# Kernel optimization log

Hardware: AMD Instinct MI355X
Metric: run time of the kernel (lower is better)

Reference implementation:

```python
import jax, jax.numpy as jnp
import numpy as np

UNITS = 512
D_Q = 1024
D_V = 1024


def setup_inputs() -> dict:
    key = jax.random.key(0)
    ks = jax.random.split(key, 12)
    B, L = 32, 2048
    inp = {
        "query": jax.random.normal(ks[0], (B, D_Q), jnp.float32),
        "values": jax.random.normal(ks[1], (B, L, D_V), jnp.float32),
        "mask": jnp.zeros((B, L, 1), jnp.float32),
        "previous_scores": jax.random.uniform(ks[2], (B, L, 1), jnp.float32),
        "timestep": 3,
        # Dense params (glorot-ish scale)
        "Wh": jax.random.normal(ks[3], (D_Q, UNITS), jnp.float32) / np.sqrt(D_Q),
        "bh": jnp.zeros((UNITS,), jnp.float32),
        "Wv": jax.random.normal(ks[4], (D_V, UNITS), jnp.float32) / np.sqrt(D_V),
        "bv": jnp.zeros((UNITS,), jnp.float32),
        "Wp": jax.random.normal(ks[5], (3, UNITS), jnp.float32) / np.sqrt(3.0),
        "bp": jnp.zeros((UNITS,), jnp.float32),
        "Wm": jax.random.normal(ks[6], (5, UNITS), jnp.float32) / np.sqrt(5.0),
        "bm": jnp.zeros((UNITS,), jnp.float32),
        "vw": jax.random.normal(ks[7], (UNITS, 1), jnp.float32) / np.sqrt(UNITS),
        "vb": jnp.zeros((1,), jnp.float32),
    }
    return inp


def reference(query, values, mask, previous_scores, timestep,
              Wh, bh, Wv, bv, Wp, bp, Wm, bm, vw, vb):
    B, L, _ = mask.shape
    # input_lengths: 1 + count of mask==0 along seq, tiled across L  -> [B, L, 1]
    input_len = 1.0 + jnp.sum((mask == 0).astype(jnp.float32), axis=1)  # [B, 1]
    input_len = jnp.broadcast_to(input_len, (B, L))[..., None]          # [B, L, 1]
    # positional features: [1+timestep, 2+pos, input_len], logged -> [B, L, 3]
    pos2 = jnp.stack([jnp.full((L,), 1.0 + timestep, jnp.float32),
                      2.0 + jnp.arange(L, dtype=jnp.float32)], axis=-1)  # [L, 2]
    pos2 = jnp.broadcast_to(pos2[None], (B, L, 2))
    positional = jnp.log(jnp.concatenate([pos2, input_len], axis=-1))    # [B, L, 3]
    # markov: sliding window of width 5 over zero-padded previous scores -> [B, L, 5]
    padded = jnp.pad(previous_scores[:, :, 0], ((0, 0), (2, 2)))         # [B, L+4]
    widx = jnp.arange(L)[:, None] + jnp.arange(5)[None, :]               # [L, 5]
    markov = padded[:, widx]                                             # [B, L, 5]
    # additive attention score
    summand = (jnp.einsum('bq,qu->bu', query, Wh) + bh)[:, None, :]      # [B, 1, U]
    summand = summand + (jnp.einsum('blv,vu->blu', values, Wv) + bv)
    summand = summand + (jnp.einsum('blp,pu->blu', positional, Wp) + bp)
    summand = summand + (jnp.einsum('blm,mu->blu', markov, Wm) + bm)
    score = jnp.einsum('blu,uo->blo', jnp.tanh(summand), vw) + vb        # [B, L, 1]
    score = score + mask * (-1e9)
    attention_weights = jax.nn.softmax(score, axis=1)                    # [B, L, 1]
    context_vector = jnp.sum(attention_weights * values, axis=1)         # [B, D_V]
    return (context_vector, attention_weights)
```

## Files before the change

kernel.cpp:

```cpp
#include <hip/hip_runtime.h>
#include <hip/hip_bf16.h>
#include <math.h>

#define NB 32
#define LL 2048
#define DV 1024
#define NU 512
#define NM (NB * LL)

typedef __attribute__((ext_vector_type(8))) short short8;
typedef __attribute__((ext_vector_type(4))) float f32x4;

#define GLL16(g, l)                                                            \
  __builtin_amdgcn_global_load_lds(                                            \
      (const __attribute__((address_space(1))) void*)(g),                      \
      (__attribute__((address_space(3))) void*)(l), 16, 0, 0)

__device__ __forceinline__ float fast_tanh(float x) {
  x = fminf(fmaxf(x, -15.f), 15.f);
  float e = __expf(2.f * x);
  return (e - 1.f) / (e + 1.f);
}

__global__ __launch_bounds__(256) void prep_kernel(
    const float* __restrict__ Wv, __hip_bfloat16* __restrict__ wvpk,
    const float* __restrict__ q, const float* __restrict__ Wh,
    const float* __restrict__ bh, const float* __restrict__ bv,
    const float* __restrict__ bp, const float* __restrict__ bm,
    const float* __restrict__ Wp, const int* __restrict__ ts,
    const float* __restrict__ mask, float* __restrict__ h) {
  if (blockIdx.x < 64) {
    int t = blockIdx.x * 256 + threadIdx.x;
    int u4 = t & 127;
    int kg = t >> 7;
    int k0 = kg * 8;
    int kt = kg >> 2;
    int qd = kg & 3;
    float4 f[8];
#pragma unroll
    for (int j = 0; j < 8; j++)
      f[j] = *(const float4*)(Wv + (size_t)(k0 + j) * NU + u4 * 4);
#pragma unroll
    for (int e = 0; e < 4; e++) {
      int u = u4 * 4 + e;
      int nt = u >> 8, n = u & 255;
      int c = qd ^ ((n >> 1) & 3);
      int idx = nt * 32768 + kt * 1024 + n * 4 + c;
      const float* fe = (const float*)&f[0] + e;
      union {
        __hip_bfloat162 h2[4];
        int4 v;
      } pk;
#pragma unroll
      for (int m = 0; m < 4; m++)
        pk.h2[m] =
            __float22bfloat162_rn(make_float2(fe[(2 * m) * 4], fe[(2 * m + 1) * 4]));
      ((int4*)wvpk)[idx] = pk.v;
    }
    return;
  }
  int idx2 = blockIdx.x - 64;
  int u0 = (idx2 & 7) * 64;
  int bq = idx2 >> 3;
  int tid = threadIdx.x;

  __shared__ float qsL[8][1024];
  __shared__ float cnt[8], lgl[8];

  {
    int g = tid & 31, bl = tid >> 5;
    const float4* mrow =
        (const float4*)(mask + (size_t)(bq * 8 + bl) * LL) + g * 16;
    float c = 0.f;
#pragma unroll
    for (int j = 0; j < 16; j++) {
      float4 m = mrow[j];
      c += (m.x == 0.f ? 1.f : 0.f) + (m.y == 0.f ? 1.f : 0.f) +
           (m.z == 0.f ? 1.f : 0.f) + (m.w == 0.f ? 1.f : 0.f);
    }
#pragma unroll
    for (int o = 16; o >= 1; o >>= 1) c += __shfl_xor(c, o, 64);
    if (g == 0) cnt[bl] = c;
  }
  __syncthreads();
  if (tid < 8) lgl[tid] = logf(1.f + cnt[tid]);

#pragma unroll
  for (int j = 0; j < 8; j++) {
    int f = j * 256 + tid;
    int bl = f >> 8, k4 = f & 255;
    *(float4*)&qsL[bl][k4 * 4] =
        *(const float4*)(q + (size_t)(bq * 8 + bl) * 1024 + k4 * 4);
  }
  __syncthreads();

  int u = tid & 63, bsub = tid >> 6;
  int b0 = bq * 8 + bsub * 2, b1 = b0 + 1;
  float a0e = 0.f, a0o = 0.f, a1e = 0.f, a1o = 0.f;
#pragma unroll 16
  for (int k = 0; k < 1024; k += 2) {
    float w0 = Wh[(size_t)k * NU + u0 + u];
    float w1 = Wh[(size_t)(k + 1) * NU + u0 + u];
    a0e += w0 * qsL[bsub * 2][k];
    a1e += w0 * qsL[bsub * 2 + 1][k];
    a0o += w1 * qsL[bsub * 2][k + 1];
    a1o += w1 * qsL[bsub * 2 + 1][k + 1];
  }
  float acc0 = a0e + a0o, acc1 = a1e + a1o;

  int uu = u0 + u;
  float lt = logf(1.0f + (float)ts[0]);
  float bias = bh[uu] + bv[uu] + bp[uu] + bm[uu] + lt * Wp[uu];
  float wp2 = Wp[2 * NU + uu];
  h[b0 * NU + uu] = acc0 + bias + lgl[bsub * 2] * wp2;
  h[b1 * NU + uu] = acc1 + bias + lgl[bsub * 2 + 1] * wp2;
}

__global__ __launch_bounds__(512, 4) void score_kernel(
    const float* __restrict__ values, const __hip_bfloat16* __restrict__ wvpk,
    const float* __restrict__ h, const float* __restrict__ Wp,
    const float* __restrict__ Wm, const float* __restrict__ vw,
    const float* __restrict__ prev, float* __restrict__ partial) {
  int lin = blockIdx.x;
  int group = lin >> 4, sub = lin & 15;
  int ntile = sub >> 3;
  int mtile = group * 8 + (sub & 7);
  int tid = threadIdx.x;
  int lane = tid & 63, wid = tid >> 6;
  int wr = wid >> 2, wc = wid & 3;
  int col = lane & 15, quad = lane >> 4;
  int b = mtile >> 4;
  int l0 = (mtile & 15) << 7;
  int rowbase = mtile << 7;

  __shared__ __align__(16) char AsB[2][8192];
  __shared__ __align__(16) char BsB[2][16384];
  __shared__ float hL[256], wp1L[256], vwL[256], wmL[5][256];
  __shared__ float loglS[128], prevs[132], scoreAcc[128];

  if (tid < 256) {
    int u = ntile * 256 + tid;
    hL[tid] = h[b * NU + u];
    wp1L[tid] = Wp[NU + u];
    vwL[tid] = vw[u];
#pragma unroll
    for (int j = 0; j < 5; j++) wmL[j][tid] = Wm[j * NU + u];
  }
  if (tid < 128) {
    loglS[tid] = __logf(2.0f + (float)(l0 + tid));
    scoreAcc[tid] = 0.f;
  }
  if (tid < 132) {
    int li = l0 - 2 + tid;
    prevs[tid] = (li >= 0 && li < LL) ? prev[(size_t)b * LL + li] : 0.f;
  }

  f32x4 acc[4][4];
  f32x4 zero4 = {0.f, 0.f, 0.f, 0.f};
#pragma unroll
  for (int i = 0; i < 4; i++)
#pragma unroll
    for (int j = 0; j < 4; j++) acc[i][j] = zero4;

  int row = tid >> 2, h0 = tid & 3;
  const float* abase = values + (size_t)(rowbase + row) * DV + h0 * 8;
  int s_sw = (row >> 1) & 3;
  int aoff = row * 64 + ((h0 ^ s_sw) * 16);
  const char* bbase = (const char*)wvpk + (size_t)ntile * 32 * 16384;
  int boff = tid * 16;

  float4 preA[2][2];

#define CVT_STORE(SLOT, DSTBUF)                                                \
  {                                                                            \
    float4 f0 = preA[SLOT][0], f1 = preA[SLOT][1];                             \
    union {                                                                    \
      __hip_bfloat162 h2[4];                                                   \
      int4 v;                                                                  \
    } pk;                                                                      \
    pk.h2[0] = __float22bfloat162_rn(make_float2(f0.x, f0.y));                 \
    pk.h2[1] = __float22bfloat162_rn(make_float2(f0.z, f0.w));                 \
    pk.h2[2] = __float22bfloat162_rn(make_float2(f1.x, f1.y));                 \
    pk.h2[3] = __float22bfloat162_rn(make_float2(f1.z, f1.w));                 \
    *(int4*)(AsB[DSTBUF] + aoff) = pk.v;                                       \
  }

  {
#pragma unroll
    for (int d = 0; d < 2; d++) {
      preA[d][0] = *(const float4*)(abase + d * 32);
      preA[d][1] = *(const float4*)(abase + d * 32 + 4);
    }
    GLL16(bbase + boff, BsB[0] + boff);
    GLL16(bbase + boff + 8192, BsB[0] + boff + 8192);
    CVT_STORE(0, 0);
    preA[0][0] = *(const float4*)(abase + 2 * 32);
    preA[0][1] = *(const float4*)(abase + 2 * 32 + 4);
    __syncthreads();
  }

#define KSTEP(KT, CBUF, OSLOT, DO_STAGE, DO_RELOAD)                            \
  {                                                                            \
    if (DO_STAGE) {                                                            \
      const char* bsrc = bbase + (size_t)((KT) + 1) * 16384;                   \
      GLL16(bsrc + boff, BsB[(CBUF) ^ 1] + boff);                              \
      GLL16(bsrc + boff + 8192, BsB[(CBUF) ^ 1] + boff + 8192);                \
      CVT_STORE(OSLOT, (CBUF) ^ 1);                                            \
      if (DO_RELOAD) {                                                         \
        preA[OSLOT][0] = *(const float4*)(abase + ((KT) + 3) * 32);            \
        preA[OSLOT][1] = *(const float4*)(abase + ((KT) + 3) * 32 + 4);        \
      }                                                                        \
    }                                                                          \
    short8 aF[4];                                                              \
    _Pragma("unroll") for (int t = 0; t < 4; t++) {                            \
      int m = wr * 64 + t * 16 + col;                                          \
      aF[t] = *(const short8*)(AsB[CBUF] + m * 64 +                            \
                               ((quad ^ ((m >> 1) & 3)) * 16));                \
    }                                                                          \
    _Pragma("unroll") for (int tc = 0; tc < 4; tc++) {                         \
      int n = wc * 64 + tc * 16 + col;                                         \
      short8 bF =                                                              \
          *(const short8*)(BsB[CBUF] + n * 64 + ((quad ^ ((n >> 1) & 3)) * 16)); \
      _Pragma("unroll") for (int tr = 0; tr < 4; tr++) acc[tr][tc] =           \
          __builtin_amdgcn_mfma_f32_16x16x32_bf16(aF[tr], bF, acc[tr][tc], 0,  \
                                                  0, 0);                       \
    }                                                                          \
    __syncthreads();                                                           \
  }

  for (int kto = 0; kto < 14; kto++) {
    KSTEP(2 * kto, 0, 1, 1, 1);
    KSTEP(2 * kto + 1, 1, 0, 1, 1);
  }
  KSTEP(28, 0, 1, 1, 1);
  KSTEP(29, 1, 0, 1, 0);
  KSTEP(30, 0, 1, 1, 0);
  KSTEP(31, 1, 0, 0, 0);
#undef KSTEP
#undef CVT_STORE

  int rb = wr * 64;
#pragma unroll
  for (int tr = 0; tr < 4; tr++) {
    float ps[4] = {0.f, 0.f, 0.f, 0.f};
#pragma unroll
    for (int tc = 0; tc < 4; tc++) {
      int uc = wc * 64 + tc * 16 + col;
      float hh = hL[uc], wp1 = wp1L[uc], vv = vwL[uc];
      float m0 = wmL[0][uc], m1 = wmL[1][uc], m2 = wmL[2][uc],
            m3 = wmL[3][uc], m4 = wmL[4][uc];
      int r0 = rb + tr * 16 + quad * 4;
#pragma unroll
      for (int i = 0; i < 4; i++) {
        int r = r0 + i;
        float e = hh + loglS[r] * wp1 + prevs[r] * m0 + prevs[r + 1] * m1 +
                  prevs[r + 2] * m2 + prevs[r + 3] * m3 + prevs[r + 4] * m4;
        float sv = acc[tr][tc][i] + e;
        ps[i] += fast_tanh(sv) * vv;
      }
    }
#pragma unroll
    for (int i = 0; i < 4; i++) {
      float v = ps[i];
      v += __shfl_xor(v, 1, 64);
      v += __shfl_xor(v, 2, 64);
      v += __shfl_xor(v, 4, 64);
      v += __shfl_xor(v, 8, 64);
      if (col == 0) atomicAdd(&scoreAcc[rb + tr * 16 + quad * 4 + i], v);
    }
  }
  __syncthreads();
  if (tid < 128)
    partial[(size_t)ntile * NM + rowbase + tid] = scoreAcc[tid];
}

__global__ __launch_bounds__(1024) void post_kernel(
    const float* __restrict__ partial, const float* __restrict__ mask,
    const float* __restrict__ values, float* __restrict__ aw,
    float* __restrict__ out) {
  int b = blockIdx.x >> 3, chunk = blockIdx.x & 7;
  int tid = threadIdx.x;
  int lane = tid & 63, wid = tid >> 6;
  __shared__ float wmx[16], wsm[16];
  __shared__ float awL[256];
  __shared__ f32x4 red[4][256];

  size_t base = (size_t)b * LL;
  float s1, s2;
  {
    size_t l1 = base + tid, l2 = base + tid + 1024;
    s1 = partial[l1] + partial[(size_t)NM + l1] + mask[l1] * -1.0e9f;
    s2 = partial[l2] + partial[(size_t)NM + l2] + mask[l2] * -1.0e9f;
  }
  float mx = fmaxf(s1, s2);
#pragma unroll
  for (int o = 32; o >= 1; o >>= 1) mx = fmaxf(mx, __shfl_xor(mx, o, 64));
  if (lane == 0) wmx[wid] = mx;
  __syncthreads();
  mx = wmx[0];
#pragma unroll
  for (int j = 1; j < 16; j++) mx = fmaxf(mx, wmx[j]);
  float e = __expf(s1 - mx) + __expf(s2 - mx);
#pragma unroll
  for (int o = 32; o >= 1; o >>= 1) e += __shfl_xor(e, o, 64);
  if (lane == 0) wsm[wid] = e;
  __syncthreads();
  float sum = 0.f;
#pragma unroll
  for (int j = 0; j < 16; j++) sum += wsm[j];
  float inv = 1.0f / sum;

  int l0 = chunk * 256;
  if (tid < 256) {
    size_t l = base + l0 + tid;
    float s = partial[l] + partial[(size_t)NM + l] + mask[l] * -1.0e9f;
    float a = __expf(s - mx) * inv;
    aw[l] = a;
    awL[tid] = a;
  }
  __syncthreads();

  int s = tid & 255, rg = tid >> 8;
  const float4* vbase =
      (const float4*)(values + ((size_t)b * LL + l0 + rg * 64) * DV) + s;
  const float* awr = awL + rg * 64;
  float4 acc = make_float4(0.f, 0.f, 0.f, 0.f);
  for (int i0 = 0; i0 < 64; i0 += 8) {
    float4 v[8];
#pragma unroll
    for (int j = 0; j < 8; j++) v[j] = vbase[(size_t)(i0 + j) * 256];
#pragma unroll
    for (int j = 0; j < 8; j++) {
      float w = awr[i0 + j];
      acc.x += w * v[j].x;
      acc.y += w * v[j].y;
      acc.z += w * v[j].z;
      acc.w += w * v[j].w;
    }
  }
  f32x4 a4 = {acc.x, acc.y, acc.z, acc.w};
  red[rg][s] = a4;
  __syncthreads();
  if (tid < 256) {
    f32x4 r = red[0][s];
    f32x4 r1 = red[1][s], r2 = red[2][s], r3 = red[3][s];
    r += r1;
    r += r2;
    r += r3;
    float* o = out + (size_t)b * DV + s * 4;
    atomicAdd(o + 0, r[0]);
    atomicAdd(o + 1, r[1]);
    atomicAdd(o + 2, r[2]);
    atomicAdd(o + 3, r[3]);
  }
}

extern "C" void kernel_launch(void* const* d_in, const int* in_sizes, int n_in,
                              void* d_out, int out_size, void* d_ws,
                              size_t ws_size, hipStream_t stream) {
  const float* query = (const float*)d_in[0];
  const float* values = (const float*)d_in[1];
  const float* mask = (const float*)d_in[2];
  const float* prev = (const float*)d_in[3];
  const int* ts = (const int*)d_in[4];
  const float* Wh = (const float*)d_in[5];
  const float* bh = (const float*)d_in[6];
  const float* Wv = (const float*)d_in[7];
  const float* bv = (const float*)d_in[8];
  const float* Wp = (const float*)d_in[9];
  const float* bp = (const float*)d_in[10];
  const float* Wm = (const float*)d_in[11];
  const float* bm = (const float*)d_in[12];
  const float* vw = (const float*)d_in[13];

  float* out = (float*)d_out;
  float* ws = (float*)d_ws;
  float* h = ws + 1024;
  float* partial = ws + 32768;
  __hip_bfloat16* wvpk =
      (__hip_bfloat16*)((char*)d_ws + (size_t)163840 * 4);
  float* aw = out + 32768;

  hipMemsetAsync(d_out, 0, 32768 * sizeof(float), stream);
  prep_kernel<<<96, 256, 0, stream>>>(Wv, wvpk, query, Wh, bh, bv, bp, bm, Wp,
                                      ts, mask, h);
  score_kernel<<<1024, 512, 0, stream>>>(values, wvpk, h, Wp, Wm, vw, prev,
                                         partial);
  post_kernel<<<256, 1024, 0, stream>>>(partial, mask, values, aw, out);
}
```

Measured before the change: 515.3 us.

## Widen score tile to all 512 units, dropping the N split and partial sums

Each score block now computes the full 512-unit output width, where before two blocks each handled 256 units. The values tile is read and converted to bf16 once instead of twice, and the score is written directly, so post_kernel no longer adds two partial arrays. The cost is double the accumulator registers (occupancy bound lowered from 4 to 2), a 64KB B double buffer in LDS, and the grid split into two launches of 256 blocks each. This may cut parallelism and latency hiding.

```diff
diff --git a/kernel.cpp b/kernel.cpp
--- a/kernel.cpp
+++ b/kernel.cpp
@@ -116,15 +116,12 @@
   h[b1 * NU + uu] = acc1 + bias + lgl[bsub * 2 + 1] * wp2;
 }
 
-__global__ __launch_bounds__(512, 4) void score_kernel(
+__global__ __launch_bounds__(512, 2) void score_kernel(
     const float* __restrict__ values, const __hip_bfloat16* __restrict__ wvpk,
     const float* __restrict__ h, const float* __restrict__ Wp,
     const float* __restrict__ Wm, const float* __restrict__ vw,
-    const float* __restrict__ prev, float* __restrict__ partial) {
-  int lin = blockIdx.x;
-  int group = lin >> 4, sub = lin & 15;
-  int ntile = sub >> 3;
-  int mtile = group * 8 + (sub & 7);
+    const float* __restrict__ prev, float* __restrict__ score, int mbase) {
+  int mtile = mbase + blockIdx.x;
   int tid = threadIdx.x;
   int lane = tid & 63, wid = tid >> 6;
   int wr = wid >> 2, wc = wid & 3;
@@ -134,17 +131,16 @@
   int rowbase = mtile << 7;
 
   __shared__ __align__(16) char AsB[2][8192];
-  __shared__ __align__(16) char BsB[2][16384];
-  __shared__ float hL[256], wp1L[256], vwL[256], wmL[5][256];
+  __shared__ __align__(16) char BsB[2][32768];
+  __shared__ float hL[512], wp1L[512], vwL[512], wmL[5][512];
   __shared__ float loglS[128], prevs[132], scoreAcc[128];
 
-  if (tid < 256) {
-    int u = ntile * 256 + tid;
-    hL[tid] = h[b * NU + u];
-    wp1L[tid] = Wp[NU + u];
-    vwL[tid] = vw[u];
-#pragma unroll
-    for (int j = 0; j < 5; j++) wmL[j][tid] = Wm[j * NU + u];
+  {
+    hL[tid] = h[b * NU + tid];
+    wp1L[tid] = Wp[NU + tid];
+    vwL[tid] = vw[tid];
+#pragma unroll
+    for (int j = 0; j < 5; j++) wmL[j][tid] = Wm[j * NU + tid];
   }
   if (tid < 128) {
     loglS[tid] = __logf(2.0f + (float)(l0 + tid));
@@ -155,18 +151,18 @@
     prevs[tid] = (li >= 0 && li < LL) ? prev[(size_t)b * LL + li] : 0.f;
   }
 
-  f32x4 acc[4][4];
+  f32x4 acc[4][8];
   f32x4 zero4 = {0.f, 0.f, 0.f, 0.f};
 #pragma unroll
   for (int i = 0; i < 4; i++)
 #pragma unroll
-    for (int j = 0; j < 4; j++) acc[i][j] = zero4;
+    for (int j = 0; j < 8; j++) acc[i][j] = zero4;
 
   int row = tid >> 2, h0 = tid & 3;
   const float* abase = values + (size_t)(rowbase + row) * DV + h0 * 8;
   int s_sw = (row >> 1) & 3;
   int aoff = row * 64 + ((h0 ^ s_sw) * 16);
-  const char* bbase = (const char*)wvpk + (size_t)ntile * 32 * 16384;
+  const char* bbase = (const char*)wvpk;
   int boff = tid * 16;
 
   float4 preA[2][2];
@@ -185,14 +181,23 @@
     *(int4*)(AsB[DSTBUF] + aoff) = pk.v;                                       \
   }
 
+#define STAGE_B(KT, DSTBUF)                                                    \
+  {                                                                            \
+    const char* s0 = bbase + (size_t)(KT) * 16384;                             \
+    const char* s1 = bbase + 524288 + (size_t)(KT) * 16384;                    \
+    GLL16(s0 + boff, BsB[DSTBUF] + boff);                                      \
+    GLL16(s0 + boff + 8192, BsB[DSTBUF] + boff + 8192);                        \
+    GLL16(s1 + boff, BsB[DSTBUF] + 16384 + boff);                              \
+    GLL16(s1 + boff + 8192, BsB[DSTBUF] + 24576 + boff);                       \
+  }
+
   {
 #pragma unroll
     for (int d = 0; d < 2; d++) {
       preA[d][0] = *(const float4*)(abase + d * 32);
       preA[d][1] = *(const float4*)(abase + d * 32 + 4);
     }
-    GLL16(bbase + boff, BsB[0] + boff);
-    GLL16(bbase + boff + 8192, BsB[0] + boff + 8192);
+    STAGE_B(0, 0);
     CVT_STORE(0, 0);
     preA[0][0] = *(const float4*)(abase + 2 * 32);
     preA[0][1] = *(const float4*)(abase + 2 * 32 + 4);
@@ -202,9 +207,7 @@
 #define KSTEP(KT, CBUF, OSLOT, DO_STAGE, DO_RELOAD)                            \
   {                                                                            \
     if (DO_STAGE) {                                                            \
-      const char* bsrc = bbase + (size_t)((KT) + 1) * 16384;                   \
-      GLL16(bsrc + boff, BsB[(CBUF) ^ 1] + boff);                              \
-      GLL16(bsrc + boff + 8192, BsB[(CBUF) ^ 1] + boff + 8192);                \
+      STAGE_B((KT) + 1, (CBUF) ^ 1);                                           \
       CVT_STORE(OSLOT, (CBUF) ^ 1);                                            \
       if (DO_RELOAD) {                                                         \
         preA[OSLOT][0] = *(const float4*)(abase + ((KT) + 3) * 32);            \
@@ -217,8 +220,8 @@
       aF[t] = *(const short8*)(AsB[CBUF] + m * 64 +                            \
                                ((quad ^ ((m >> 1) & 3)) * 16));                \
     }                                                                          \
-    _Pragma("unroll") for (int tc = 0; tc < 4; tc++) {                         \
-      int n = wc * 64 + tc * 16 + col;                                         \
+    _Pragma("unroll") for (int tc = 0; tc < 8; tc++) {                         \
+      int n = wc * 128 + tc * 16 + col;                                        \
       short8 bF =                                                              \
           *(const short8*)(BsB[CBUF] + n * 64 + ((quad ^ ((n >> 1) & 3)) * 16)); \
       _Pragma("unroll") for (int tr = 0; tr < 4; tr++) acc[tr][tc] =           \
@@ -237,6 +240,7 @@
   KSTEP(30, 0, 1, 1, 0);
   KSTEP(31, 1, 0, 0, 0);
 #undef KSTEP
+#undef STAGE_B
 #undef CVT_STORE
 
   int rb = wr * 64;
@@ -244,8 +248,8 @@
   for (int tr = 0; tr < 4; tr++) {
     float ps[4] = {0.f, 0.f, 0.f, 0.f};
 #pragma unroll
-    for (int tc = 0; tc < 4; tc++) {
-      int uc = wc * 64 + tc * 16 + col;
+    for (int tc = 0; tc < 8; tc++) {
+      int uc = wc * 128 + tc * 16 + col;
       float hh = hL[uc], wp1 = wp1L[uc], vv = vwL[uc];
       float m0 = wmL[0][uc], m1 = wmL[1][uc], m2 = wmL[2][uc],
             m3 = wmL[3][uc], m4 = wmL[4][uc];
@@ -270,12 +274,11 @@
     }
   }
   __syncthreads();
-  if (tid < 128)
-    partial[(size_t)ntile * NM + rowbase + tid] = scoreAcc[tid];
+  if (tid < 128) score[rowbase + tid] = scoreAcc[tid];
 }
 
 __global__ __launch_bounds__(1024) void post_kernel(
-    const float* __restrict__ partial, const float* __restrict__ mask,
+    const float* __restrict__ score, const float* __restrict__ mask,
     const float* __restrict__ values, float* __restrict__ aw,
     float* __restrict__ out) {
   int b = blockIdx.x >> 3, chunk = blockIdx.x & 7;
@@ -289,8 +292,8 @@
   float s1, s2;
   {
     size_t l1 = base + tid, l2 = base + tid + 1024;
-    s1 = partial[l1] + partial[(size_t)NM + l1] + mask[l1] * -1.0e9f;
-    s2 = partial[l2] + partial[(size_t)NM + l2] + mask[l2] * -1.0e9f;
+    s1 = score[l1] + mask[l1] * -1.0e9f;
+    s2 = score[l2] + mask[l2] * -1.0e9f;
   }
   float mx = fmaxf(s1, s2);
 #pragma unroll
@@ -313,7 +316,7 @@
   int l0 = chunk * 256;
   if (tid < 256) {
     size_t l = base + l0 + tid;
-    float s = partial[l] + partial[(size_t)NM + l] + mask[l] * -1.0e9f;
+    float s = score[l] + mask[l] * -1.0e9f;
     float a = __expf(s - mx) * inv;
     aw[l] = a;
     awL[tid] = a;
@@ -376,7 +379,7 @@
   float* out = (float*)d_out;
   float* ws = (float*)d_ws;
   float* h = ws + 1024;
-  float* partial = ws + 32768;
+  float* score = ws + 32768;
   __hip_bfloat16* wvpk =
       (__hip_bfloat16*)((char*)d_ws + (size_t)163840 * 4);
   float* aw = out + 32768;
@@ -384,7 +387,9 @@
   hipMemsetAsync(d_out, 0, 32768 * sizeof(float), stream);
   prep_kernel<<<96, 256, 0, stream>>>(Wv, wvpk, query, Wh, bh, bv, bp, bm, Wp,
                                       ts, mask, h);
-  score_kernel<<<1024, 512, 0, stream>>>(values, wvpk, h, Wp, Wm, vw, prev,
-                                         partial);
-  post_kernel<<<256, 1024, 0, stream>>>(partial, mask, values, aw, out);
-}
+  score_kernel<<<256, 512, 0, stream>>>(values, wvpk, h, Wp, Wm, vw, prev,
+                                        score, 0);
+  score_kernel<<<256, 512, 0, stream>>>(values, wvpk, h, Wp, Wm, vw, prev,
+                                        score, 256);
+  post_kernel<<<256, 1024, 0, stream>>>(score, mask, values, aw, out);
+}
```

Measured after the change: 538.5 us. 4.5% more time.
